# Performance work log

Measured on AMD Instinct MI355X. Metric: run time of the kernel, lower is better.

## Reference

```python
import jax, jax.numpy as jnp
import numpy as np

# Thresholds from PointsGeneration.__init__ defaults
THRES_TEXT = 0.45
THRES_HEAD = 0.5
THRES_BOND = 0.5

H = W = 2048


def setup_inputs() -> dict:
    key = jax.random.key(0)
    ks = jax.random.split(key, 7)
    mk = lambda k, c: jax.random.normal(k, (1, c, H, W), dtype=jnp.float32)
    return {
        "score_text": mk(ks[0], 1),
        "score_head": mk(ks[1], 1),
        "score_tail": mk(ks[2], 1),
        "score_bond": mk(ks[3], 1),
        "reg_head": mk(ks[4], 4),
        "reg_tail": mk(ks[5], 4),
        "reg_bond": mk(ks[6], 4),
    }


def reference(score_text, score_head, score_tail, score_bond, reg_head, reg_tail, reg_bond):
    # Sigmoid activations (exactly as in torch forward).
    s_text = jax.nn.sigmoid(score_text)
    s_head = jax.nn.sigmoid(score_head)
    s_tail = jax.nn.sigmoid(score_tail)
    s_bond = jax.nn.sigmoid(score_bond)

    # Per-pixel thresholding performed by the .so before per-instance point
    # generation: center-text mask, head/tail masks (within text region),
    # pixels passing the corresponding mask, so we gate them here.
    m_text = (s_text > THRES_TEXT).astype(s_text.dtype)   # [1,1,H,W]
    m_head = m_text * (s_head > THRES_HEAD).astype(s_head.dtype)
    m_tail = m_text * (s_tail > THRES_HEAD).astype(s_tail.dtype)
    m_bond = (s_bond > THRES_BOND).astype(s_bond.dtype)

    gated = jnp.concatenate([
        reg_head * m_head,   # [1,4,H,W]
        reg_tail * m_tail,   # [1,4,H,W]
        reg_bond * m_bond,   # [1,4,H,W]
    ], axis=1)

    return jnp.concatenate([s_text, s_head, s_tail, s_bond, gated], axis=1)
```

## Files before the change

### kernel.cpp

```cpp
#include <hip/hip_runtime.h>
#include <math.h>


typedef float f32x4 __attribute__((ext_vector_type(4)));

static __device__ __forceinline__ float sigf(float x) {
    return 1.0f / (1.0f + expf(-x));
}

static __device__ __forceinline__ f32x4 ldnt4(const float* p) {
    return __builtin_nontemporal_load(reinterpret_cast<const f32x4*>(p));
}
static __device__ __forceinline__ void stnt4(float* p, f32x4 v) {
    __builtin_nontemporal_store(v, reinterpret_cast<f32x4*>(p));
}

__global__ __launch_bounds__(256) void points_gen_kernel(
    const float* __restrict__ p_text,
    const float* __restrict__ p_head,
    const float* __restrict__ p_tail,
    const float* __restrict__ p_bond,
    const float* __restrict__ p_rh,
    const float* __restrict__ p_rt,
    const float* __restrict__ p_rb,
    float* __restrict__ out)
{
    constexpr int N = 2048 * 2048;
    const int t = blockIdx.x * blockDim.x + threadIdx.x;
    const int i = t * 4;

    f32x4 st = ldnt4(p_text + i);
    f32x4 sh = ldnt4(p_head + i);
    f32x4 sl = ldnt4(p_tail + i);
    f32x4 sb = ldnt4(p_bond + i);

    f32x4 mh, ml, mb;
#pragma unroll
    for (int k = 0; k < 4; ++k) {
        st[k] = sigf(st[k]);
        sh[k] = sigf(sh[k]);
        sl[k] = sigf(sl[k]);
        sb[k] = sigf(sb[k]);
        const float mt = (st[k] > 0.45f) ? 1.0f : 0.0f;
        mh[k] = (sh[k] > 0.5f) ? mt : 0.0f;
        ml[k] = (sl[k] > 0.5f) ? mt : 0.0f;
        mb[k] = (sb[k] > 0.5f) ? 1.0f : 0.0f;
    }

    stnt4(out + 0 * N + i, st);
    stnt4(out + 1 * N + i, sh);
    stnt4(out + 2 * N + i, sl);
    stnt4(out + 3 * N + i, sb);

#pragma unroll
    for (int c = 0; c < 4; ++c) {
        f32x4 v = ldnt4(p_rh + c * N + i);
        v *= mh;
        stnt4(out + (4 + c) * N + i, v);
    }
#pragma unroll
    for (int c = 0; c < 4; ++c) {
        f32x4 v = ldnt4(p_rt + c * N + i);
        v *= ml;
        stnt4(out + (8 + c) * N + i, v);
    }
#pragma unroll
    for (int c = 0; c < 4; ++c) {
        f32x4 v = ldnt4(p_rb + c * N + i);
        v *= mb;
        stnt4(out + (12 + c) * N + i, v);
    }
}

extern "C" void kernel_launch(void* const* d_in, const int* in_sizes, int n_in,
                              void* d_out, int out_size, void* d_ws, size_t ws_size,
                              hipStream_t stream) {
    (void)in_sizes; (void)n_in; (void)out_size; (void)d_ws; (void)ws_size;

    const float* p_text = (const float*)d_in[0];
    const float* p_head = (const float*)d_in[1];
    const float* p_tail = (const float*)d_in[2];
    const float* p_bond = (const float*)d_in[3];
    const float* p_rh   = (const float*)d_in[4];
    const float* p_rt   = (const float*)d_in[5];
    const float* p_rb   = (const float*)d_in[6];
    float* out = (float*)d_out;

    constexpr int N = 2048 * 2048;
    constexpr int threads = 256;
    constexpr int n4 = N / 4;
    constexpr int blocks = n4 / threads;

    points_gen_kernel<<<blocks, threads, 0, stream>>>(
        p_text, p_head, p_tail, p_bond, p_rh, p_rt, p_rb, out);
}
```

Baseline: 122.3 us.

## Process 2048 pixels per wave with batched loads and bitmask gating

Each wave now handles 2048 contiguous pixels, with each thread issuing 8 vector loads per channel before computing, which raises memory-level parallelism and cuts the grid eightfold. Nontemporal loads and stores are replaced with ordinary ones. Masks are packed into 32-bit bitmasks and applied with selects instead of multiplies. The cost is higher register pressure, and possibly lower occupancy, from holding 32 float4 vectors per thread.

After: 107.5 us. 1.14x faster.

```diff
diff --git a/kernel.cpp b/kernel.cpp
--- a/kernel.cpp
+++ b/kernel.cpp
@@ -8,11 +8,11 @@
     return 1.0f / (1.0f + expf(-x));
 }
 
-static __device__ __forceinline__ f32x4 ldnt4(const float* p) {
-    return __builtin_nontemporal_load(reinterpret_cast<const f32x4*>(p));
+static __device__ __forceinline__ f32x4 ld4(const float* p) {
+    return *reinterpret_cast<const f32x4*>(p);
 }
-static __device__ __forceinline__ void stnt4(float* p, f32x4 v) {
-    __builtin_nontemporal_store(v, reinterpret_cast<f32x4*>(p));
+static __device__ __forceinline__ void st4(float* p, f32x4 v) {
+    *reinterpret_cast<f32x4*>(p) = v;
 }
 
 __global__ __launch_bounds__(256) void points_gen_kernel(
@@ -26,49 +26,107 @@
     float* __restrict__ out)
 {
     constexpr int N = 2048 * 2048;
-    const int t = blockIdx.x * blockDim.x + threadIdx.x;
-    const int i = t * 4;
+    constexpr int WPX = 2048;
+    const int lane = threadIdx.x & 63;
+    const int wave = (blockIdx.x * blockDim.x + threadIdx.x) >> 6;
+    const int base = wave * WPX + lane * 4;
 
-    f32x4 st = ldnt4(p_text + i);
-    f32x4 sh = ldnt4(p_head + i);
-    f32x4 sl = ldnt4(p_tail + i);
-    f32x4 sb = ldnt4(p_bond + i);
+    f32x4 T[8], H[8], L[8], B[8];
+#pragma unroll
+    for (int j = 0; j < 8; ++j) T[j] = ld4(p_text + base + j * 256);
+#pragma unroll
+    for (int j = 0; j < 8; ++j) H[j] = ld4(p_head + base + j * 256);
+#pragma unroll
+    for (int j = 0; j < 8; ++j) L[j] = ld4(p_tail + base + j * 256);
+#pragma unroll
+    for (int j = 0; j < 8; ++j) B[j] = ld4(p_bond + base + j * 256);
 
-    f32x4 mh, ml, mb;
+    unsigned mt = 0, mh = 0, ml = 0, mb = 0;
 #pragma unroll
-    for (int k = 0; k < 4; ++k) {
-        st[k] = sigf(st[k]);
-        sh[k] = sigf(sh[k]);
-        sl[k] = sigf(sl[k]);
-        sb[k] = sigf(sb[k]);
-        const float mt = (st[k] > 0.45f) ? 1.0f : 0.0f;
-        mh[k] = (sh[k] > 0.5f) ? mt : 0.0f;
-        ml[k] = (sl[k] > 0.5f) ? mt : 0.0f;
-        mb[k] = (sb[k] > 0.5f) ? 1.0f : 0.0f;
+    for (int j = 0; j < 8; ++j) {
+#pragma unroll
+        for (int k = 0; k < 4; ++k) {
+            T[j][k] = sigf(T[j][k]);
+            if (T[j][k] > 0.45f) mt |= 1u << (4 * j + k);
+        }
     }
+#pragma unroll
+    for (int j = 0; j < 8; ++j) st4(out + 0 * N + base + j * 256, T[j]);
 
-    stnt4(out + 0 * N + i, st);
-    stnt4(out + 1 * N + i, sh);
-    stnt4(out + 2 * N + i, sl);
-    stnt4(out + 3 * N + i, sb);
+#pragma unroll
+    for (int j = 0; j < 8; ++j) {
+#pragma unroll
+        for (int k = 0; k < 4; ++k) {
+            H[j][k] = sigf(H[j][k]);
+            if (H[j][k] > 0.5f) mh |= 1u << (4 * j + k);
+        }
+    }
+#pragma unroll
+    for (int j = 0; j < 8; ++j) st4(out + 1 * N + base + j * 256, H[j]);
+
+#pragma unroll
+    for (int j = 0; j < 8; ++j) {
+#pragma unroll
+        for (int k = 0; k < 4; ++k) {
+            L[j][k] = sigf(L[j][k]);
+            if (L[j][k] > 0.5f) ml |= 1u << (4 * j + k);
+        }
+    }
+#pragma unroll
+    for (int j = 0; j < 8; ++j) st4(out + 2 * N + base + j * 256, L[j]);
+
+#pragma unroll
+    for (int j = 0; j < 8; ++j) {
+#pragma unroll
+        for (int k = 0; k < 4; ++k) {
+            B[j][k] = sigf(B[j][k]);
+            if (B[j][k] > 0.5f) mb |= 1u << (4 * j + k);
+        }
+    }
+#pragma unroll
+    for (int j = 0; j < 8; ++j) st4(out + 3 * N + base + j * 256, B[j]);
+
+    mh &= mt;
+    ml &= mt;
 
 #pragma unroll
     for (int c = 0; c < 4; ++c) {
-        f32x4 v = ldnt4(p_rh + c * N + i);
-        v *= mh;
-        stnt4(out + (4 + c) * N + i, v);
+        f32x4 v[8];
+#pragma unroll
+        for (int j = 0; j < 8; ++j) v[j] = ld4(p_rh + c * N + base + j * 256);
+#pragma unroll
+        for (int j = 0; j < 8; ++j)
+#pragma unroll
+            for (int k = 0; k < 4; ++k)
+                v[j][k] = (mh >> (4 * j + k)) & 1u ? v[j][k] : 0.0f;
+#pragma unroll
+        for (int j = 0; j < 8; ++j) st4(out + (4 + c) * N + base + j * 256, v[j]);
     }
 #pragma unroll
     for (int c = 0; c < 4; ++c) {
-        f32x4 v = ldnt4(p_rt + c * N + i);
-        v *= ml;
-        stnt4(out + (8 + c) * N + i, v);
+        f32x4 v[8];
+#pragma unroll
+        for (int j = 0; j < 8; ++j) v[j] = ld4(p_rt + c * N + base + j * 256);
+#pragma unroll
+        for (int j = 0; j < 8; ++j)
+#pragma unroll
+            for (int k = 0; k < 4; ++k)
+                v[j][k] = (ml >> (4 * j + k)) & 1u ? v[j][k] : 0.0f;
+#pragma unroll
+        for (int j = 0; j < 8; ++j) st4(out + (8 + c) * N + base + j * 256, v[j]);
     }
 #pragma unroll
     for (int c = 0; c < 4; ++c) {
-        f32x4 v = ldnt4(p_rb + c * N + i);
-        v *= mb;
-        stnt4(out + (12 + c) * N + i, v);
+        f32x4 v[8];
+#pragma unroll
+        for (int j = 0; j < 8; ++j) v[j] = ld4(p_rb + c * N + base + j * 256);
+#pragma unroll
+        for (int j = 0; j < 8; ++j)
+#pragma unroll
+            for (int k = 0; k < 4; ++k)
+                v[j][k] = (mb >> (4 * j + k)) & 1u ? v[j][k] : 0.0f;
+#pragma unroll
+        for (int j = 0; j < 8; ++j) st4(out + (12 + c) * N + base + j * 256, v[j]);
     }
 }
 
@@ -87,9 +145,10 @@
     float* out = (float*)d_out;
 
     constexpr int N = 2048 * 2048;
+    constexpr int WPX = 2048;
+    constexpr int waves = N / WPX;
     constexpr int threads = 256;
-    constexpr int n4 = N / 4;
-    constexpr int blocks = n4 / threads;
+    constexpr int blocks = waves * 64 / threads;
 
     points_gen_kernel<<<blocks, threads, 0, stream>>>(
         p_text, p_head, p_tail, p_bond, p_rh, p_rt, p_rb, out);
```

## Process 4096-pixel tiles per wave with bitmask masks and plain loads

Applied to the files above, without the earlier changes.

Each wave now handles a contiguous 4096-pixel tile, with each thread issuing 16 vector loads per plane before computing. Threshold masks are packed into 64-bit bitmasks and reused across regression planes. Nontemporal loads and stores are replaced with ordinary ones. This aims to raise memory-level parallelism, at the cost of higher register use, fewer blocks and different cache behaviour.

Result: faster. 113.5 us (-7.2%).

```diff
diff --git a/kernel.cpp b/kernel.cpp
--- a/kernel.cpp
+++ b/kernel.cpp
@@ -3,16 +3,56 @@
 
 
 typedef float f32x4 __attribute__((ext_vector_type(4)));
+typedef unsigned long long u64;
 
 static __device__ __forceinline__ float sigf(float x) {
     return 1.0f / (1.0f + expf(-x));
 }
 
-static __device__ __forceinline__ f32x4 ldnt4(const float* p) {
-    return __builtin_nontemporal_load(reinterpret_cast<const f32x4*>(p));
+static __device__ __forceinline__ f32x4 ld4(const float* p) {
+    return *reinterpret_cast<const f32x4*>(p);
 }
-static __device__ __forceinline__ void stnt4(float* p, f32x4 v) {
-    __builtin_nontemporal_store(v, reinterpret_cast<f32x4*>(p));
+static __device__ __forceinline__ void st4(float* p, f32x4 v) {
+    *reinterpret_cast<f32x4*>(p) = v;
+}
+
+static __device__ __forceinline__ u64 score_plane(
+    const float* __restrict__ src, float* __restrict__ dst,
+    float thr, int base)
+{
+    f32x4 V[16];
+#pragma unroll
+    for (int j = 0; j < 16; ++j) V[j] = ld4(src + base + j * 256);
+    u64 m = 0;
+#pragma unroll
+    for (int j = 0; j < 16; ++j) {
+#pragma unroll
+        for (int k = 0; k < 4; ++k) {
+            V[j][k] = sigf(V[j][k]);
+            if (V[j][k] > thr) m |= 1ull << (4 * j + k);
+        }
+    }
+#pragma unroll
+    for (int j = 0; j < 16; ++j) st4(dst + base + j * 256, V[j]);
+    return m;
+}
+
+static __device__ __forceinline__ void reg_plane(
+    const float* __restrict__ src, float* __restrict__ dst,
+    u64 m, int base)
+{
+    f32x4 V[16];
+#pragma unroll
+    for (int j = 0; j < 16; ++j) V[j] = ld4(src + base + j * 256);
+#pragma unroll
+    for (int j = 0; j < 16; ++j) {
+#pragma unroll
+        for (int k = 0; k < 4; ++k) {
+            V[j][k] = ((m >> (4 * j + k)) & 1ull) ? V[j][k] : 0.0f;
+        }
+    }
+#pragma unroll
+    for (int j = 0; j < 16; ++j) st4(dst + base + j * 256, V[j]);
 }
 
 __global__ __launch_bounds__(256) void points_gen_kernel(
@@ -26,50 +66,25 @@
     float* __restrict__ out)
 {
     constexpr int N = 2048 * 2048;
-    const int t = blockIdx.x * blockDim.x + threadIdx.x;
-    const int i = t * 4;
+    constexpr int WPX = 4096;
+    const int lane = threadIdx.x & 63;
+    const int wave = (blockIdx.x * blockDim.x + threadIdx.x) >> 6;
+    const int base = wave * WPX + lane * 4;
 
-    f32x4 st = ldnt4(p_text + i);
-    f32x4 sh = ldnt4(p_head + i);
-    f32x4 sl = ldnt4(p_tail + i);
-    f32x4 sb = ldnt4(p_bond + i);
-
-    f32x4 mh, ml, mb;
-#pragma unroll
-    for (int k = 0; k < 4; ++k) {
-        st[k] = sigf(st[k]);
-        sh[k] = sigf(sh[k]);
-        sl[k] = sigf(sl[k]);
-        sb[k] = sigf(sb[k]);
-        const float mt = (st[k] > 0.45f) ? 1.0f : 0.0f;
-        mh[k] = (sh[k] > 0.5f) ? mt : 0.0f;
-        ml[k] = (sl[k] > 0.5f) ? mt : 0.0f;
-        mb[k] = (sb[k] > 0.5f) ? 1.0f : 0.0f;
-    }
-
-    stnt4(out + 0 * N + i, st);
-    stnt4(out + 1 * N + i, sh);
-    stnt4(out + 2 * N + i, sl);
-    stnt4(out + 3 * N + i, sb);
+    const u64 mt = score_plane(p_text, out + 0 * N, 0.45f, base);
+    const u64 mh = score_plane(p_head, out + 1 * N, 0.50f, base) & mt;
+    const u64 ml = score_plane(p_tail, out + 2 * N, 0.50f, base) & mt;
+    const u64 mb = score_plane(p_bond, out + 3 * N, 0.50f, base);
 
 #pragma unroll
-    for (int c = 0; c < 4; ++c) {
-        f32x4 v = ldnt4(p_rh + c * N + i);
-        v *= mh;
-        stnt4(out + (4 + c) * N + i, v);
-    }
+    for (int c = 0; c < 4; ++c)
+        reg_plane(p_rh + c * N, out + (4 + c) * N, mh, base);
 #pragma unroll
-    for (int c = 0; c < 4; ++c) {
-        f32x4 v = ldnt4(p_rt + c * N + i);
-        v *= ml;
-        stnt4(out + (8 + c) * N + i, v);
-    }
+    for (int c = 0; c < 4; ++c)
+        reg_plane(p_rt + c * N, out + (8 + c) * N, ml, base);
 #pragma unroll
-    for (int c = 0; c < 4; ++c) {
-        f32x4 v = ldnt4(p_rb + c * N + i);
-        v *= mb;
-        stnt4(out + (12 + c) * N + i, v);
-    }
+    for (int c = 0; c < 4; ++c)
+        reg_plane(p_rb + c * N, out + (12 + c) * N, mb, base);
 }
 
 extern "C" void kernel_launch(void* const* d_in, const int* in_sizes, int n_in,
@@ -87,9 +102,10 @@
     float* out = (float*)d_out;
 
     constexpr int N = 2048 * 2048;
+    constexpr int WPX = 4096;
+    constexpr int waves = N / WPX;
     constexpr int threads = 256;
-    constexpr int n4 = N / 4;
-    constexpr int blocks = n4 / threads;
+    constexpr int blocks = waves * 64 / threads;
 
     points_gen_kernel<<<blocks, threads, 0, stream>>>(
         p_text, p_head, p_tail, p_bond, p_rh, p_rt, p_rb, out);
```
